# Kernel tuning notes

Hardware: AMD Instinct MI355X
Metric: run time of the kernel (lower is better)

Reference implementation:

```python
import jax, jax.numpy as jnp
import numpy as np

H, BOTTLENECK, TOPK = 2048, 64, 128
TAU, EPS = 1.0, 1e-20

def setup_inputs() -> dict:
    key = jax.random.key(0)
    ks = jax.random.split(key, 7)
    B, T = 4, 4096
    x = jax.random.normal(ks[0], (B, T, H), dtype=jnp.float32)
    Wd = jax.random.normal(ks[1], (H, BOTTLENECK), dtype=jnp.float32) / np.sqrt(H)
    bd = jax.random.normal(ks[2], (BOTTLENECK,), dtype=jnp.float32) * 0.01
    Wu = jax.random.normal(ks[3], (BOTTLENECK, H), dtype=jnp.float32) / np.sqrt(BOTTLENECK)
    bu = jax.random.normal(ks[4], (H,), dtype=jnp.float32) * 0.01
    Wg = jax.random.normal(ks[5], (H,), dtype=jnp.float32) / np.sqrt(H)
    bg = jax.random.normal(ks[6], (), dtype=jnp.float32) * 0.01
    return {"x": x, "Wd": Wd, "bd": bd, "Wu": Wu, "bu": bu, "Wg": Wg, "bg": bg}

def reference(x, Wd, bd, Wu, bu, Wg, bg):
    B, T, _ = x.shape
    k = max(1, min(T, TOPK))
    # gate logits: Linear(H,1).squeeze(-1) -> [B, T]
    logits = jnp.einsum('bth,h->bt', x, Wg) + bg
    # gumbel noise (fixed key for determinism; non-differentiated like torch)
    U = jax.random.uniform(jax.random.key(42), logits.shape, dtype=logits.dtype)
    g = -jnp.log(-jnp.log(U + EPS) + EPS)
    probs = jax.nn.softmax((logits + g) / TAU, axis=-1)            # [B, T]
    topk_idx = jax.lax.top_k(logits, k)[1]                          # [B, k]
    hard = jnp.zeros_like(logits).at[jnp.arange(B)[:, None], topk_idx].set(1.0)
    mask = jax.lax.stop_gradient(hard - probs) + probs              # straight-through
    # bottleneck adapter
    delta = jnp.maximum(x @ Wd + bd, 0.0) @ Wu + bu                 # [B, T, H]
    return x + delta * mask[..., None]
```

## Files before the change

kernel.cpp:

```cpp
#include <hip/hip_runtime.h>
#include <hip/hip_bf16.h>

#define H 2048
#define BN 64
#define TT 4096
#define BB 4
#define KK 128

__global__ __launch_bounds__(256) void copy_logits_kernel(
    const float* __restrict__ x, const float* __restrict__ Wg,
    const float* __restrict__ bg, float* __restrict__ out,
    float* __restrict__ logits, int nrows) {
    int row  = (blockIdx.x * blockDim.x + threadIdx.x) >> 6;
    int lane = threadIdx.x & 63;
    if (row >= nrows) return;
    const float4* x4 = (const float4*)(x + (size_t)row * H);
    float4*       o4 = (float4*)(out + (size_t)row * H);
    const float4* w4 = (const float4*)Wg;
    float acc = 0.f;
#pragma unroll
    for (int i = 0; i < 8; ++i) {
        float4 a = x4[lane + 64 * i];
        float4 b = w4[lane + 64 * i];
        o4[lane + 64 * i] = a;
        acc += a.x * b.x + a.y * b.y + a.z * b.z + a.w * b.w;
    }
#pragma unroll
    for (int off = 32; off > 0; off >>= 1) acc += __shfl_down(acc, off);
    if (lane == 0) logits[row] = acc + bg[0];
}

__global__ __launch_bounds__(256) void topk_idx_kernel(
    const float* __restrict__ logits, int* __restrict__ idxlist) {
    __shared__ unsigned keys[TT];
    __shared__ int wsum[4];
    __shared__ int gtp[256], eqp[256];
    const int tid = threadIdx.x;
    const int b   = blockIdx.x;
    const float* lr = logits + (size_t)b * TT;

    for (int i = tid; i < TT; i += 256) {
        unsigned u = __float_as_uint(lr[i]);
        keys[i] = (u & 0x80000000u) ? ~u : (u | 0x80000000u);
    }
    __syncthreads();

    unsigned prefix = 0;
    int k = KK;
    for (int bit = 31; bit >= 0; --bit) {
        unsigned ref = (prefix >> bit) | 1u;
        int c = 0;
        for (int i = tid; i < TT; i += 256) c += ((keys[i] >> bit) == ref);
#pragma unroll
        for (int off = 32; off > 0; off >>= 1) c += __shfl_down(c, off);
        if ((tid & 63) == 0) wsum[tid >> 6] = c;
        __syncthreads();
        int total = wsum[0] + wsum[1] + wsum[2] + wsum[3];
        __syncthreads();
        if (total >= k) prefix |= (1u << bit);
        else            k -= total;
    }

    const int per = TT / 256, i0 = tid * per, i1 = i0 + per;
    int cgt = 0, ceq = 0;
    for (int i = i0; i < i1; ++i) {
        cgt += (keys[i] > prefix);
        ceq += (keys[i] == prefix);
    }
    gtp[tid] = cgt; eqp[tid] = ceq;
    __syncthreads();
    if (tid == 0) {
        int sg = 0, se = 0;
        for (int t = 0; t < 256; ++t) {
            int a = gtp[t]; gtp[t] = sg; sg += a;
            int c = eqp[t]; eqp[t] = se; se += c;
        }
        wsum[0] = sg;
    }
    __syncthreads();
    const int total_gt = wsum[0];
    const int need_eq  = KK - total_gt;
    int g = gtp[tid], e = eqp[tid];
    int* dst = idxlist + b * KK;
    for (int i = i0; i < i1; ++i) {
        if (keys[i] > prefix)       dst[g++] = b * TT + i;
        else if (keys[i] == prefix) { if (e < need_eq) dst[total_gt + e] = b * TT + i; e++; }
    }
}

__global__ __launch_bounds__(256) void adapter_kernel(
    const float* __restrict__ x, const float* __restrict__ Wd,
    const float* __restrict__ bd, const float* __restrict__ Wu,
    const float* __restrict__ bu, const int* __restrict__ idxlist,
    float* __restrict__ out) {
    const int row = idxlist[blockIdx.x];
    const int tid = threadIdx.x;
    const float* xr = x + (size_t)row * H;
    float* orow     = out + (size_t)row * H;

    __shared__ float xs[H];
    __shared__ float hp[4][BN];
    __shared__ float hs[BN];

    ((float4*)xs)[tid]       = ((const float4*)xr)[tid];
    ((float4*)xs)[tid + 256] = ((const float4*)xr)[tid + 256];
    __syncthreads();

    const int j = tid & 63, g = tid >> 6;
    {
        float acc = 0.f;
        const float* wd = Wd + (size_t)(g * (H / 4)) * BN + j;
        const float* xg = xs + g * (H / 4);
#pragma unroll 8
        for (int h = 0; h < H / 4; ++h) acc += xg[h] * wd[(size_t)h * BN];
        hp[g][j] = acc;
    }
    __syncthreads();
    if (tid < BN) {
        float v = hp[0][tid] + hp[1][tid] + hp[2][tid] + hp[3][tid] + bd[tid];
        hs[tid] = v > 0.f ? v : 0.f;
    }
    __syncthreads();

    float y[8];
#pragma unroll
    for (int r = 0; r < 8; ++r) y[r] = bu[tid + 256 * r];
    for (int jj = 0; jj < BN; ++jj) {
        float hv = hs[jj];
        const float* wu = Wu + (size_t)jj * H;
#pragma unroll
        for (int r = 0; r < 8; ++r) y[r] += hv * wu[tid + 256 * r];
    }
#pragma unroll
    for (int r = 0; r < 8; ++r) orow[tid + 256 * r] = xs[tid + 256 * r] + y[r];
}

extern "C" void kernel_launch(void* const* d_in, const int* in_sizes, int n_in,
                              void* d_out, int out_size, void* d_ws, size_t ws_size,
                              hipStream_t stream) {
    const float* x  = (const float*)d_in[0];
    const float* Wd = (const float*)d_in[1];
    const float* bd = (const float*)d_in[2];
    const float* Wu = (const float*)d_in[3];
    const float* bu = (const float*)d_in[4];
    const float* Wg = (const float*)d_in[5];
    const float* bg = (const float*)d_in[6];
    float* out = (float*)d_out;

    const int nrows = in_sizes[0] / H;
    float* logits = (float*)d_ws;
    int*   idxlist = (int*)((char*)d_ws + (size_t)nrows * sizeof(float));

    copy_logits_kernel<<<(nrows + 3) / 4, 256, 0, stream>>>(x, Wg, bg, out, logits, nrows);
    topk_idx_kernel<<<BB, 256, 0, stream>>>(logits, idxlist);
    adapter_kernel<<<BB * KK, 256, 0, stream>>>(x, Wd, bd, Wu, bu, idxlist, out);
}
```

Before: 114.6 us.

## Grid-stride the copy/logit kernel and batch four rows per adapter block

The copy+gate-logit kernel becomes a fixed 1024-block grid-stride loop that keeps Wg in registers, splits the dot product across four FMA accumulators, and no longer adds the scalar bias bg (top-k ordering does not depend on it). The adapter kernel now handles four selected rows per 512-thread block, so each Wd and Wu element loaded is reused across four rows. The down-projection broadcasts x with readlane instead of staging it in shared memory, and the up-projection uses float4 loads of Wu. This cuts weight traffic and launch count in exchange for fewer blocks in the adapter stage and higher register pressure.

```diff
diff --git a/kernel.cpp b/kernel.cpp
--- a/kernel.cpp
+++ b/kernel.cpp
@@ -6,28 +6,40 @@
 #define TT 4096
 #define BB 4
 #define KK 128
+#define CP_BLOCKS 1024
+#define RPB 4
 
 __global__ __launch_bounds__(256) void copy_logits_kernel(
     const float* __restrict__ x, const float* __restrict__ Wg,
-    const float* __restrict__ bg, float* __restrict__ out,
-    float* __restrict__ logits, int nrows) {
-    int row  = (blockIdx.x * blockDim.x + threadIdx.x) >> 6;
-    int lane = threadIdx.x & 63;
-    if (row >= nrows) return;
-    const float4* x4 = (const float4*)(x + (size_t)row * H);
-    float4*       o4 = (float4*)(out + (size_t)row * H);
+    float* __restrict__ out, float* __restrict__ logits, int nrows) {
+    const int lane   = threadIdx.x & 63;
+    const int wave   = (blockIdx.x * 256 + threadIdx.x) >> 6;
+    const int nwaves = CP_BLOCKS * 4;
     const float4* w4 = (const float4*)Wg;
-    float acc = 0.f;
-#pragma unroll
-    for (int i = 0; i < 8; ++i) {
-        float4 a = x4[lane + 64 * i];
-        float4 b = w4[lane + 64 * i];
-        o4[lane + 64 * i] = a;
-        acc += a.x * b.x + a.y * b.y + a.z * b.z + a.w * b.w;
-    }
-#pragma unroll
-    for (int off = 32; off > 0; off >>= 1) acc += __shfl_down(acc, off);
-    if (lane == 0) logits[row] = acc + bg[0];
+    float4 w[8];
+#pragma unroll
+    for (int i = 0; i < 8; ++i) w[i] = w4[lane + 64 * i];
+
+    for (int row = wave; row < nrows; row += nwaves) {
+        const float4* x4 = (const float4*)(x + (size_t)row * H);
+        float4*       o4 = (float4*)(out + (size_t)row * H);
+        float4 a[8];
+#pragma unroll
+        for (int i = 0; i < 8; ++i) a[i] = x4[lane + 64 * i];
+        float s0 = 0.f, s1 = 0.f, s2 = 0.f, s3 = 0.f;
+#pragma unroll
+        for (int i = 0; i < 8; ++i) {
+            o4[lane + 64 * i] = a[i];
+            s0 = fmaf(a[i].x, w[i].x, s0);
+            s1 = fmaf(a[i].y, w[i].y, s1);
+            s2 = fmaf(a[i].z, w[i].z, s2);
+            s3 = fmaf(a[i].w, w[i].w, s3);
+        }
+        float acc = (s0 + s1) + (s2 + s3);
+#pragma unroll
+        for (int off = 32; off > 0; off >>= 1) acc += __shfl_down(acc, off);
+        if (lane == 0) logits[row] = acc;
+    }
 }
 
 __global__ __launch_bounds__(256) void topk_idx_kernel(
@@ -88,51 +100,84 @@
     }
 }
 
-__global__ __launch_bounds__(256) void adapter_kernel(
+__global__ __launch_bounds__(512) void adapter_kernel(
     const float* __restrict__ x, const float* __restrict__ Wd,
     const float* __restrict__ bd, const float* __restrict__ Wu,
     const float* __restrict__ bu, const int* __restrict__ idxlist,
     float* __restrict__ out) {
-    const int row = idxlist[blockIdx.x];
-    const int tid = threadIdx.x;
-    const float* xr = x + (size_t)row * H;
-    float* orow     = out + (size_t)row * H;
-
-    __shared__ float xs[H];
-    __shared__ float hp[4][BN];
-    __shared__ float hs[BN];
-
-    ((float4*)xs)[tid]       = ((const float4*)xr)[tid];
-    ((float4*)xs)[tid + 256] = ((const float4*)xr)[tid + 256];
-    __syncthreads();
-
-    const int j = tid & 63, g = tid >> 6;
+    __shared__ float hp[8][RPB][BN];
+    __shared__ float hs[RPB][BN];
+    const int tid  = threadIdx.x;
+    const int lane = tid & 63;
+    const int g    = tid >> 6;
+
+    int rows[RPB];
+#pragma unroll
+    for (int r = 0; r < RPB; ++r) rows[r] = idxlist[blockIdx.x * RPB + r];
+
+    float xr0[4], xr1[4], xr2[4], xr3[4];
     {
-        float acc = 0.f;
-        const float* wd = Wd + (size_t)(g * (H / 4)) * BN + j;
-        const float* xg = xs + g * (H / 4);
+        const float* p0 = x + (size_t)rows[0] * H + g * 256 + lane;
+        const float* p1 = x + (size_t)rows[1] * H + g * 256 + lane;
+        const float* p2 = x + (size_t)rows[2] * H + g * 256 + lane;
+        const float* p3 = x + (size_t)rows[3] * H + g * 256 + lane;
+#pragma unroll
+        for (int k = 0; k < 4; ++k) {
+            xr0[k] = p0[k * 64]; xr1[k] = p1[k * 64];
+            xr2[k] = p2[k * 64]; xr3[k] = p3[k * 64];
+        }
+    }
+
+    float a0 = 0.f, a1 = 0.f, a2 = 0.f, a3 = 0.f;
+    const float* wdp = Wd + (size_t)(g * 256) * BN + lane;
+#pragma unroll
+    for (int k = 0; k < 4; ++k) {
 #pragma unroll 8
-        for (int h = 0; h < H / 4; ++h) acc += xg[h] * wd[(size_t)h * BN];
-        hp[g][j] = acc;
-    }
-    __syncthreads();
-    if (tid < BN) {
-        float v = hp[0][tid] + hp[1][tid] + hp[2][tid] + hp[3][tid] + bd[tid];
-        hs[tid] = v > 0.f ? v : 0.f;
-    }
-    __syncthreads();
-
-    float y[8];
-#pragma unroll
-    for (int r = 0; r < 8; ++r) y[r] = bu[tid + 256 * r];
+        for (int l = 0; l < 64; ++l) {
+            float wv = wdp[(size_t)(k * 64 + l) * BN];
+            a0 = fmaf(__int_as_float(__builtin_amdgcn_readlane(__float_as_int(xr0[k]), l)), wv, a0);
+            a1 = fmaf(__int_as_float(__builtin_amdgcn_readlane(__float_as_int(xr1[k]), l)), wv, a1);
+            a2 = fmaf(__int_as_float(__builtin_amdgcn_readlane(__float_as_int(xr2[k]), l)), wv, a2);
+            a3 = fmaf(__int_as_float(__builtin_amdgcn_readlane(__float_as_int(xr3[k]), l)), wv, a3);
+        }
+    }
+    hp[g][0][lane] = a0; hp[g][1][lane] = a1;
+    hp[g][2][lane] = a2; hp[g][3][lane] = a3;
+    __syncthreads();
+
+    if (tid < RPB * BN) {
+        int r = tid >> 6, jj = tid & 63;
+        float v = bd[jj];
+#pragma unroll
+        for (int gg = 0; gg < 8; ++gg) v += hp[gg][r][jj];
+        hs[r][jj] = v > 0.f ? v : 0.f;
+    }
+    __syncthreads();
+
+    const float4* Wu4 = (const float4*)Wu;
+    float4 y0 = ((const float4*)bu)[tid];
+    float4 y1 = y0, y2 = y0, y3 = y0;
     for (int jj = 0; jj < BN; ++jj) {
-        float hv = hs[jj];
-        const float* wu = Wu + (size_t)jj * H;
-#pragma unroll
-        for (int r = 0; r < 8; ++r) y[r] += hv * wu[tid + 256 * r];
-    }
-#pragma unroll
-    for (int r = 0; r < 8; ++r) orow[tid + 256 * r] = xs[tid + 256 * r] + y[r];
+        float4 wv = Wu4[(size_t)jj * (H / 4) + tid];
+        float h0 = hs[0][jj], h1 = hs[1][jj], h2 = hs[2][jj], h3 = hs[3][jj];
+        y0.x = fmaf(h0, wv.x, y0.x); y0.y = fmaf(h0, wv.y, y0.y);
+        y0.z = fmaf(h0, wv.z, y0.z); y0.w = fmaf(h0, wv.w, y0.w);
+        y1.x = fmaf(h1, wv.x, y1.x); y1.y = fmaf(h1, wv.y, y1.y);
+        y1.z = fmaf(h1, wv.z, y1.z); y1.w = fmaf(h1, wv.w, y1.w);
+        y2.x = fmaf(h2, wv.x, y2.x); y2.y = fmaf(h2, wv.y, y2.y);
+        y2.z = fmaf(h2, wv.z, y2.z); y2.w = fmaf(h2, wv.w, y2.w);
+        y3.x = fmaf(h3, wv.x, y3.x); y3.y = fmaf(h3, wv.y, y3.y);
+        y3.z = fmaf(h3, wv.z, y3.z); y3.w = fmaf(h3, wv.w, y3.w);
+    }
+
+#pragma unroll
+    for (int r = 0; r < RPB; ++r) {
+        const float4* xr4 = (const float4*)(x + (size_t)rows[r] * H);
+        float4*       o4  = (float4*)(out + (size_t)rows[r] * H);
+        float4 xa = xr4[tid];
+        float4 yv = (r == 0) ? y0 : (r == 1) ? y1 : (r == 2) ? y2 : y3;
+        o4[tid] = make_float4(xa.x + yv.x, xa.y + yv.y, xa.z + yv.z, xa.w + yv.w);
+    }
 }
 
 extern "C" void kernel_launch(void* const* d_in, const int* in_sizes, int n_in,
@@ -144,14 +189,13 @@
     const float* Wu = (const float*)d_in[3];
     const float* bu = (const float*)d_in[4];
     const float* Wg = (const float*)d_in[5];
-    const float* bg = (const float*)d_in[6];
     float* out = (float*)d_out;
 
     const int nrows = in_sizes[0] / H;
-    float* logits = (float*)d_ws;
+    float* logits  = (float*)d_ws;
     int*   idxlist = (int*)((char*)d_ws + (size_t)nrows * sizeof(float));
 
-    copy_logits_kernel<<<(nrows + 3) / 4, 256, 0, stream>>>(x, Wg, bg, out, logits, nrows);
+    copy_logits_kernel<<<CP_BLOCKS, 256, 0, stream>>>(x, Wg, out, logits, nrows);
     topk_idx_kernel<<<BB, 256, 0, stream>>>(logits, idxlist);
-    adapter_kernel<<<BB * KK, 256, 0, stream>>>(x, Wd, bd, Wu, bu, idxlist, out);
-}
+    adapter_kernel<<<(BB * KK) / RPB, 512, 0, stream>>>(x, Wd, bd, Wu, bu, idxlist, out);
+}
```

Result: faster. 102.2 us (-10.8%).
